# Kernel optimization log

Measured on AMD Instinct MI355X. Metric: run time of the kernel, lower is better.

The kernel has to match this reference:

```python
import jax, jax.numpy as jnp
import numpy as np

TOP_K = 2


def setup_inputs() -> dict:
    key = jax.random.key(0)
    k1, k2, k3, k4, k5 = jax.random.split(key, 5)
    H, F, E = 1024, 2048, 8
    B, S = 2, 1024
    return {
        "hidden_states": jax.random.normal(k1, (B, S, H), dtype=jnp.float32),
        "gate_w": jax.random.normal(k2, (E, H), dtype=jnp.float32) * (1.0 / np.sqrt(H)),
        "w1": jax.random.normal(k3, (E, F, H), dtype=jnp.float32) * (1.0 / np.sqrt(H)),
        "w2": jax.random.normal(k4, (E, H, F), dtype=jnp.float32) * (1.0 / np.sqrt(F)),
        "w3": jax.random.normal(k5, (E, F, H), dtype=jnp.float32) * (1.0 / np.sqrt(H)),
    }


def reference(hidden_states, gate_w, w1, w2, w3):
    B, S, H = hidden_states.shape
    E = gate_w.shape[0]
    x = hidden_states.reshape(-1, H)  # [T, H]

    # Router: softmax in float32, top-k, renormalize (exact Mixtral math)
    router_logits = x @ gate_w.T  # [T, E]
    probs = jax.nn.softmax(router_logits.astype(jnp.float32), axis=-1)
    routing_weights, selected = jax.lax.top_k(probs, TOP_K)  # [T, K]
    routing_weights = routing_weights / routing_weights.sum(axis=-1, keepdims=True)
    routing_weights = routing_weights.astype(x.dtype)

    # Per-token combine weight for each expert: [T, E]
    combine = (jax.nn.one_hot(selected, E, dtype=x.dtype) * routing_weights[..., None]).sum(axis=1)

    # Dense grouped expert SwiGLU MLP (zero combine weight for unselected experts
    # makes this strictly equivalent to the gathered/dispatched computation)
    h = jnp.einsum('th,efh->etf', x, w1)   # [E, T, F]
    g = jnp.einsum('th,efh->etf', x, w3)   # [E, T, F]
    mid = jax.nn.silu(h) * g               # SwiGLU
    expert_out = jnp.einsum('etf,ehf->eth', mid, w2)  # [E, T, H]
    out = jnp.einsum('eth,te->th', expert_out, combine)  # weighted combine

    return out.reshape(B, S, H), router_logits
```

## Files before the change

kernel.cpp:

```cpp
#include <hip/hip_runtime.h>
#include <hip/hip_bf16.h>
#include <math.h>

#define H 1024
#define FF 2048
#define E 8
#define T 2048
#define NSLOT (2*T)
#define SLOT_PAD 128

typedef __attribute__((ext_vector_type(8))) short s16x8;
typedef __attribute__((ext_vector_type(4))) float f32x4;
typedef __attribute__((ext_vector_type(4))) unsigned int u32x4;

static __device__ __forceinline__ unsigned short f2bf(float f) {
    union { float f; unsigned u; } v; v.f = f;
    unsigned r = v.u + 0x7fff + ((v.u >> 16) & 1);
    return (unsigned short)(r >> 16);
}
static __device__ __forceinline__ float bf2f(unsigned short s) {
    union { unsigned u; float f; } v; v.u = ((unsigned)s) << 16;
    return v.f;
}
static __device__ __forceinline__ unsigned pack2(float a, float b) {
    return (unsigned)f2bf(a) | ((unsigned)f2bf(b) << 16);
}

static __device__ __forceinline__ s16x8 cvt8(f32x4 lo, f32x4 hi) {
    union { u32x4 u; s16x8 s; } r;
    asm("v_cvt_pk_bf16_f32 %0, %1, %2" : "=v"(r.u.x) : "v"(lo.x), "v"(lo.y));
    asm("v_cvt_pk_bf16_f32 %0, %1, %2" : "=v"(r.u.y) : "v"(lo.z), "v"(lo.w));
    asm("v_cvt_pk_bf16_f32 %0, %1, %2" : "=v"(r.u.z) : "v"(hi.x), "v"(hi.y));
    asm("v_cvt_pk_bf16_f32 %0, %1, %2" : "=v"(r.u.w) : "v"(hi.z), "v"(hi.w));
    return r.s;
}

typedef __attribute__((address_space(3))) unsigned int lds_uint;
typedef const __attribute__((address_space(1))) unsigned int glob_uint;
static __device__ __forceinline__ void gl_lds16(const void* g, void* l) {
    __builtin_amdgcn_global_load_lds((glob_uint*)g, (lds_uint*)l, 16, 0, 0);
}

static __device__ __forceinline__ void expert_range(const int* __restrict__ counts,
                                                    int e, int& off, int& cnt) {
    int acc = 0;
    #pragma unroll
    for (int i = 0; i < E; ++i) {
        int c = counts[i];
        if (i < e) acc += c;
        if (i == e) cnt = c;
    }
    off = acc;
}

__global__ __launch_bounds__(256) void router_kernel(
    const float* __restrict__ x, const float* __restrict__ gw,
    unsigned short* __restrict__ xb,
    float* __restrict__ logits_out, int* __restrict__ top_id,
    float* __restrict__ top_w, int* __restrict__ counts)
{
    int t = blockIdx.x;
    int tid = threadIdx.x;
    const float* xr = x + (size_t)t * H;
    {
        f32x4 v = *(const f32x4*)(xr + tid * 4);
        uint2 rr; rr.x = pack2(v.x, v.y); rr.y = pack2(v.z, v.w);
        *(uint2*)(xb + (size_t)t * H + tid * 4) = rr;
    }
    int e = tid >> 5;
    int l32 = tid & 31;
    const float* gr = gw + (size_t)e * H;
    float s = 0.f;
    for (int h = l32; h < H; h += 32) s += xr[h] * gr[h];
    for (int off = 16; off; off >>= 1) s += __shfl_down(s, off, 32);
    __shared__ float lg[E];
    if (l32 == 0) lg[e] = s;
    __syncthreads();
    if (tid < E) logits_out[(size_t)t * E + tid] = lg[tid];
    if (tid == 0) {
        int i1 = 0; float b1 = lg[0];
        for (int i = 1; i < E; ++i) if (lg[i] > b1) { b1 = lg[i]; i1 = i; }
        int i2 = -1; float b2 = -INFINITY;
        for (int i = 0; i < E; ++i) if (i != i1 && lg[i] > b2) { b2 = lg[i]; i2 = i; }
        float p2 = expf(b2 - b1);
        float inv = 1.f / (1.f + p2);
        top_id[2*t]   = i1;  top_id[2*t+1] = i2;
        top_w[2*t]    = inv; top_w[2*t+1]  = p2 * inv;
        atomicAdd(&counts[i1], 1);
        atomicAdd(&counts[i2], 1);
    }
}

__global__ __launch_bounds__(256) void assign_kernel(
    const int* __restrict__ top_id, const int* __restrict__ counts,
    int* __restrict__ cursors, int* __restrict__ top_pos,
    int* __restrict__ slot_token)
{
    int t = blockIdx.x * 256 + threadIdx.x;
    if (t >= T) return;
    int offs[E];
    {
        int acc = 0;
        #pragma unroll
        for (int i = 0; i < E; ++i) { offs[i] = acc; acc += counts[i]; }
    }
    #pragma unroll
    for (int k = 0; k < 2; ++k) {
        int e = top_id[2*t + k];
        int p = offs[e] + atomicAdd(&cursors[e], 1);
        top_pos[2*t + k] = p;
        slot_token[p] = t;
    }
}

__global__ __launch_bounds__(256) void gemm1_kernel(
    const unsigned short* __restrict__ xb, const int* __restrict__ slot_token,
    const float* __restrict__ w1f, const float* __restrict__ w3f,
    const int* __restrict__ counts, unsigned short* __restrict__ mid)
{
    int e = blockIdx.z;
    int off, cnt;
    expert_range(counts, e, off, cnt);
    int m0 = blockIdx.y * 128;
    if (m0 >= cnt) return;
    int f0 = blockIdx.x * 128;

    __shared__ __align__(16) unsigned short sx[128 * 64];
    __shared__ __align__(16) float s1f[128 * 64];
    __shared__ __align__(16) float s3f[128 * 64];

    int tid = threadIdx.x;
    int wv = tid >> 6, ln = tid & 63;
    int quad = ln >> 4, l16 = ln & 15;
    int wm = wv & 1, wn = wv >> 1;
    int xor7 = l16 & 7;

    const unsigned short* xsrc[4]; unsigned short* xdst[4];
    #pragma unroll
    for (int j = 0; j < 4; ++j) {
        int row = wv * 32 + j * 8 + (ln >> 3);
        int slot = off + m0 + row;
        if (m0 + row >= cnt) slot = off;
        int tok = slot_token[slot];
        int cl = (ln & 7) ^ (row & 7);
        xsrc[j] = xb + (size_t)tok * H + cl * 8;
        xdst[j] = &sx[(wv * 32 + j * 8) * 64];
    }
    const float *b1src[8], *b3src[8]; float *b1dst[8], *b3dst[8];
    #pragma unroll
    for (int j = 0; j < 8; ++j) {
        int row = wv * 32 + j * 4 + (ln >> 4);
        int g = (ln & 15) ^ (row & 15);
        b1src[j] = w1f + ((size_t)e * FF + f0 + row) * H + g * 4;
        b3src[j] = w3f + ((size_t)e * FF + f0 + row) * H + g * 4;
        b1dst[j] = &s1f[(wv * 32 + j * 4) * 64];
        b3dst[j] = &s3f[(wv * 32 + j * 4) * 64];
    }

    f32x4 acc1[4][4], acc3[4][4];
    #pragma unroll
    for (int i = 0; i < 4; ++i)
        #pragma unroll
        for (int j = 0; j < 4; ++j) {
            acc1[i][j] = (f32x4){0.f, 0.f, 0.f, 0.f};
            acc3[i][j] = (f32x4){0.f, 0.f, 0.f, 0.f};
        }

    for (int k0 = 0; k0 < H; k0 += 64) {
        #pragma unroll
        for (int j = 0; j < 4; ++j) gl_lds16(xsrc[j] + k0, xdst[j]);
        #pragma unroll
        for (int j = 0; j < 8; ++j) {
            gl_lds16(b1src[j] + k0, b1dst[j]);
            gl_lds16(b3src[j] + k0, b3dst[j]);
        }
        __syncthreads();
        #pragma unroll
        for (int ks = 0; ks < 2; ++ks) {
            int qa  = (quad + 4 * ks) ^ xor7;
            int cph = qa << 3;
            int p2  = (quad + 4 * ks) << 1;
            s16x8 a[4], b1v[4], b3v[4];
            #pragma unroll
            for (int i = 0; i < 4; ++i)
                a[i] = *(const s16x8*)&sx[(wm * 64 + i * 16 + l16) * 64 + cph];
            #pragma unroll
            for (int j = 0; j < 4; ++j) {
                int rb = (wn * 64 + j * 16 + l16) * 64;
                int g0 = (p2 ^ l16) << 2;
                int g1 = ((p2 ^ 1) ^ l16) << 2;
                b1v[j] = cvt8(*(const f32x4*)&s1f[rb + g0], *(const f32x4*)&s1f[rb + g1]);
                b3v[j] = cvt8(*(const f32x4*)&s3f[rb + g0], *(const f32x4*)&s3f[rb + g1]);
            }
            #pragma unroll
            for (int i = 0; i < 4; ++i)
                #pragma unroll
                for (int j = 0; j < 4; ++j) {
                    acc1[i][j] = __builtin_amdgcn_mfma_f32_16x16x32_bf16(a[i], b1v[j], acc1[i][j], 0, 0, 0);
                    acc3[i][j] = __builtin_amdgcn_mfma_f32_16x16x32_bf16(a[i], b3v[j], acc3[i][j], 0, 0, 0);
                }
        }
        __syncthreads();
    }

    #pragma unroll
    for (int i = 0; i < 4; ++i) {
        #pragma unroll
        for (int r = 0; r < 4; ++r) {
            int row = wm * 64 + i * 16 + quad * 4 + r;
            if (m0 + row < cnt) {
                size_t base = (size_t)(off + m0 + row) * FF + f0 + wn * 64;
                #pragma unroll
                for (int j = 0; j < 4; ++j) {
                    float h = acc1[i][j][r];
                    float g = acc3[i][j][r];
                    float v = h / (1.f + __expf(-h)) * g;
                    mid[base + j * 16 + l16] = f2bf(v);
                }
            }
        }
    }
}

__global__ __launch_bounds__(256) void gemm2_kernel(
    const unsigned short* __restrict__ mid, const float* __restrict__ w2f,
    const int* __restrict__ counts, unsigned short* __restrict__ y)
{
    int e = blockIdx.z;
    int off, cnt;
    expert_range(counts, e, off, cnt);
    int m0 = blockIdx.y * 128;
    if (m0 >= cnt) return;
    int n0 = blockIdx.x * 128;

    __shared__ __align__(16) unsigned short sa[128 * 64];
    __shared__ __align__(16) float sbf[128 * 64];

    int tid = threadIdx.x;
    int wv = tid >> 6, ln = tid & 63;
    int quad = ln >> 4, l16 = ln & 15;
    int wm = wv & 1, wn = wv >> 1;
    int xor7 = l16 & 7;

    const unsigned short* asrc[4]; unsigned short* adst[4];
    #pragma unroll
    for (int j = 0; j < 4; ++j) {
        int row = wv * 32 + j * 8 + (ln >> 3);
        int cl = (ln & 7) ^ (row & 7);
        asrc[j] = mid + (size_t)(off + m0 + row) * FF + cl * 8;
        adst[j] = &sa[(wv * 32 + j * 8) * 64];
    }
    const float* bsrc[8]; float* bdst[8];
    #pragma unroll
    for (int j = 0; j < 8; ++j) {
        int row = wv * 32 + j * 4 + (ln >> 4);
        int g = (ln & 15) ^ (row & 15);
        bsrc[j] = w2f + ((size_t)e * H + n0 + row) * FF + g * 4;
        bdst[j] = &sbf[(wv * 32 + j * 4) * 64];
    }

    f32x4 acc[4][4];
    #pragma unroll
    for (int i = 0; i < 4; ++i)
        #pragma unroll
        for (int j = 0; j < 4; ++j) acc[i][j] = (f32x4){0.f, 0.f, 0.f, 0.f};

    for (int k0 = 0; k0 < FF; k0 += 64) {
        #pragma unroll
        for (int j = 0; j < 4; ++j) gl_lds16(asrc[j] + k0, adst[j]);
        #pragma unroll
        for (int j = 0; j < 8; ++j) gl_lds16(bsrc[j] + k0, bdst[j]);
        __syncthreads();
        #pragma unroll
        for (int ks = 0; ks < 2; ++ks) {
            int qa  = (quad + 4 * ks) ^ xor7;
            int cph = qa << 3;
            int p2  = (quad + 4 * ks) << 1;
            s16x8 a[4], b[4];
            #pragma unroll
            for (int i = 0; i < 4; ++i)
                a[i] = *(const s16x8*)&sa[(wm * 64 + i * 16 + l16) * 64 + cph];
            #pragma unroll
            for (int j = 0; j < 4; ++j) {
                int rb = (wn * 64 + j * 16 + l16) * 64;
                int g0 = (p2 ^ l16) << 2;
                int g1 = ((p2 ^ 1) ^ l16) << 2;
                b[j] = cvt8(*(const f32x4*)&sbf[rb + g0], *(const f32x4*)&sbf[rb + g1]);
            }
            #pragma unroll
            for (int i = 0; i < 4; ++i)
                #pragma unroll
                for (int j = 0; j < 4; ++j)
                    acc[i][j] = __builtin_amdgcn_mfma_f32_16x16x32_bf16(a[i], b[j], acc[i][j], 0, 0, 0);
        }
        __syncthreads();
    }

    #pragma unroll
    for (int i = 0; i < 4; ++i) {
        #pragma unroll
        for (int r = 0; r < 4; ++r) {
            int row = wm * 64 + i * 16 + quad * 4 + r;
            if (m0 + row < cnt) {
                size_t base = (size_t)(off + m0 + row) * H + n0 + wn * 64;
                #pragma unroll
                for (int j = 0; j < 4; ++j)
                    y[base + j * 16 + l16] = f2bf(acc[i][j][r]);
            }
        }
    }
}

__global__ __launch_bounds__(256) void combine_kernel(
    const unsigned short* __restrict__ y, const int* __restrict__ top_pos,
    const float* __restrict__ top_w, float* __restrict__ out)
{
    int t = blockIdx.x, tid = threadIdx.x;
    int p0 = top_pos[2*t], p1 = top_pos[2*t+1];
    float w0 = top_w[2*t], w1 = top_w[2*t+1];
    ushort4 a = ((const ushort4*)(y + (size_t)p0 * H))[tid];
    ushort4 b = ((const ushort4*)(y + (size_t)p1 * H))[tid];
    float4 o;
    o.x = w0 * bf2f(a.x) + w1 * bf2f(b.x);
    o.y = w0 * bf2f(a.y) + w1 * bf2f(b.y);
    o.z = w0 * bf2f(a.z) + w1 * bf2f(b.z);
    o.w = w0 * bf2f(a.w) + w1 * bf2f(b.w);
    ((float4*)(out + (size_t)t * H))[tid] = o;
}

extern "C" void kernel_launch(void* const* d_in, const int* in_sizes, int n_in,
                              void* d_out, int out_size, void* d_ws, size_t ws_size,
                              hipStream_t stream) {
    const float* x  = (const float*)d_in[0];
    const float* gw = (const float*)d_in[1];
    const float* w1 = (const float*)d_in[2];
    const float* w2 = (const float*)d_in[3];
    const float* w3 = (const float*)d_in[4];
    float* out    = (float*)d_out;
    float* logits = out + (size_t)T * H;

    int* counts      = (int*)d_ws;
    int* cursors     = counts + 8;
    int* top_id      = counts + 16;
    int* top_pos     = top_id + 2*T;
    int* slot_token  = top_pos + 2*T;
    float* top_w     = (float*)(slot_token + NSLOT);
    unsigned short* xb  = (unsigned short*)(top_w + 2*T);
    unsigned short* mid = xb  + (size_t)T * H;
    unsigned short* y   = mid + (size_t)(NSLOT + SLOT_PAD) * FF;

    (void)hipMemsetAsync(counts, 0, 16 * sizeof(int), stream);

    router_kernel<<<T, 256, 0, stream>>>(x, gw, xb, logits, top_id, top_w, counts);
    assign_kernel<<<(T + 255) / 256, 256, 0, stream>>>(top_id, counts, cursors,
                                                       top_pos, slot_token);
    gemm1_kernel<<<dim3(FF / 128, 16, E), 256, 0, stream>>>(xb, slot_token,
                                                            w1, w3, counts, mid);
    gemm2_kernel<<<dim3(H / 128, 16, E), 256, 0, stream>>>(mid, w2, counts, y);
    combine_kernel<<<T, 256, 0, stream>>>(y, top_pos, top_w, out);
}
```

Before: 436.1 us.

## Fuse combine into gemm2 via atomic scatter and split-K over two halves

Removes the separate combine kernel and the bf16 y intermediate. gemm2 now scales each output row by its routing weight and atomically adds it into the zeroed fp32 output at the owning token's row. The K dimension of gemm2 is split in two, doubling the grid for better occupancy. In exchange it adds a memset of the output, many fp32 atomics with contention, and a summation order that is no longer deterministic.

```diff
diff --git a/kernel.cpp b/kernel.cpp
--- a/kernel.cpp
+++ b/kernel.cpp
@@ -93,8 +93,9 @@
 
 __global__ __launch_bounds__(256) void assign_kernel(
     const int* __restrict__ top_id, const int* __restrict__ counts,
-    int* __restrict__ cursors, int* __restrict__ top_pos,
-    int* __restrict__ slot_token)
+    const float* __restrict__ top_w,
+    int* __restrict__ cursors, int* __restrict__ slot_token,
+    float* __restrict__ slot_w)
 {
     int t = blockIdx.x * 256 + threadIdx.x;
     if (t >= T) return;
@@ -108,8 +109,8 @@
     for (int k = 0; k < 2; ++k) {
         int e = top_id[2*t + k];
         int p = offs[e] + atomicAdd(&cursors[e], 1);
-        top_pos[2*t + k] = p;
         slot_token[p] = t;
+        slot_w[p] = top_w[2*t + k];
     }
 }
 
@@ -224,14 +225,17 @@
 
 __global__ __launch_bounds__(256) void gemm2_kernel(
     const unsigned short* __restrict__ mid, const float* __restrict__ w2f,
-    const int* __restrict__ counts, unsigned short* __restrict__ y)
+    const int* __restrict__ counts, const int* __restrict__ slot_token,
+    const float* __restrict__ slot_w, float* __restrict__ out)
 {
-    int e = blockIdx.z;
+    int e  = blockIdx.z >> 1;
+    int ks2 = blockIdx.z & 1;
     int off, cnt;
     expert_range(counts, e, off, cnt);
     int m0 = blockIdx.y * 128;
     if (m0 >= cnt) return;
     int n0 = blockIdx.x * 128;
+    int kbase = ks2 * (FF / 2);
 
     __shared__ __align__(16) unsigned short sa[128 * 64];
     __shared__ __align__(16) float sbf[128 * 64];
@@ -247,7 +251,7 @@
     for (int j = 0; j < 4; ++j) {
         int row = wv * 32 + j * 8 + (ln >> 3);
         int cl = (ln & 7) ^ (row & 7);
-        asrc[j] = mid + (size_t)(off + m0 + row) * FF + cl * 8;
+        asrc[j] = mid + (size_t)(off + m0 + row) * FF + kbase + cl * 8;
         adst[j] = &sa[(wv * 32 + j * 8) * 64];
     }
     const float* bsrc[8]; float* bdst[8];
@@ -255,7 +259,7 @@
     for (int j = 0; j < 8; ++j) {
         int row = wv * 32 + j * 4 + (ln >> 4);
         int g = (ln & 15) ^ (row & 15);
-        bsrc[j] = w2f + ((size_t)e * H + n0 + row) * FF + g * 4;
+        bsrc[j] = w2f + ((size_t)e * H + n0 + row) * FF + kbase + g * 4;
         bdst[j] = &sbf[(wv * 32 + j * 4) * 64];
     }
 
@@ -265,7 +269,7 @@
         #pragma unroll
         for (int j = 0; j < 4; ++j) acc[i][j] = (f32x4){0.f, 0.f, 0.f, 0.f};
 
-    for (int k0 = 0; k0 < FF; k0 += 64) {
+    for (int k0 = 0; k0 < FF / 2; k0 += 64) {
         #pragma unroll
         for (int j = 0; j < 4; ++j) gl_lds16(asrc[j] + k0, adst[j]);
         #pragma unroll
@@ -302,30 +306,16 @@
         for (int r = 0; r < 4; ++r) {
             int row = wm * 64 + i * 16 + quad * 4 + r;
             if (m0 + row < cnt) {
-                size_t base = (size_t)(off + m0 + row) * H + n0 + wn * 64;
+                int slot = off + m0 + row;
+                int tok = slot_token[slot];
+                float w = slot_w[slot];
+                float* orow = out + (size_t)tok * H + n0 + wn * 64;
                 #pragma unroll
                 for (int j = 0; j < 4; ++j)
-                    y[base + j * 16 + l16] = f2bf(acc[i][j][r]);
+                    atomicAdd(&orow[j * 16 + l16], w * acc[i][j][r]);
             }
         }
     }
-}
-
-__global__ __launch_bounds__(256) void combine_kernel(
-    const unsigned short* __restrict__ y, const int* __restrict__ top_pos,
-    const float* __restrict__ top_w, float* __restrict__ out)
-{
-    int t = blockIdx.x, tid = threadIdx.x;
-    int p0 = top_pos[2*t], p1 = top_pos[2*t+1];
-    float w0 = top_w[2*t], w1 = top_w[2*t+1];
-    ushort4 a = ((const ushort4*)(y + (size_t)p0 * H))[tid];
-    ushort4 b = ((const ushort4*)(y + (size_t)p1 * H))[tid];
-    float4 o;
-    o.x = w0 * bf2f(a.x) + w1 * bf2f(b.x);
-    o.y = w0 * bf2f(a.y) + w1 * bf2f(b.y);
-    o.z = w0 * bf2f(a.z) + w1 * bf2f(b.z);
-    o.w = w0 * bf2f(a.w) + w1 * bf2f(b.w);
-    ((float4*)(out + (size_t)t * H))[tid] = o;
 }
 
 extern "C" void kernel_launch(void* const* d_in, const int* in_sizes, int n_in,
@@ -342,20 +332,20 @@
     int* counts      = (int*)d_ws;
     int* cursors     = counts + 8;
     int* top_id      = counts + 16;
-    int* top_pos     = top_id + 2*T;
-    int* slot_token  = top_pos + 2*T;
+    int* slot_token  = top_id + 2*T;
     float* top_w     = (float*)(slot_token + NSLOT);
-    unsigned short* xb  = (unsigned short*)(top_w + 2*T);
+    float* slot_w    = top_w + 2*T;
+    unsigned short* xb  = (unsigned short*)(slot_w + NSLOT);
     unsigned short* mid = xb  + (size_t)T * H;
-    unsigned short* y   = mid + (size_t)(NSLOT + SLOT_PAD) * FF;
 
     (void)hipMemsetAsync(counts, 0, 16 * sizeof(int), stream);
+    (void)hipMemsetAsync(out, 0, (size_t)T * H * sizeof(float), stream);
 
     router_kernel<<<T, 256, 0, stream>>>(x, gw, xb, logits, top_id, top_w, counts);
-    assign_kernel<<<(T + 255) / 256, 256, 0, stream>>>(top_id, counts, cursors,
-                                                       top_pos, slot_token);
+    assign_kernel<<<(T + 255) / 256, 256, 0, stream>>>(top_id, counts, top_w,
+                                                       cursors, slot_token, slot_w);
     gemm1_kernel<<<dim3(FF / 128, 16, E), 256, 0, stream>>>(xb, slot_token,
                                                             w1, w3, counts, mid);
-    gemm2_kernel<<<dim3(H / 128, 16, E), 256, 0, stream>>>(mid, w2, counts, y);
-    combine_kernel<<<T, 256, 0, stream>>>(y, top_pos, top_w, out);
-}
+    gemm2_kernel<<<dim3(H / 128, 16, E * 2), 256, 0, stream>>>(mid, w2, counts,
+                                                               slot_token, slot_w, out);
+}
```

New measurement: 451.2 us. +3.5%, slower.
